# Optimization experiments

Measured on AMD Instinct MI355X. Metric: run time of the kernel, lower is better.

Reference implementation:

```python
import jax, jax.numpy as jnp
import numpy as np

NM, ND, E, H, HEADS = 1043, 2166, 512, 512, 8
EMM, EDD = 66752, 138624


def setup_inputs() -> dict:
    ks = iter(jax.random.split(jax.random.key(0), 64))
    def nk():
        return next(ks)
    s = 0.05
    inp = {
        'mirna_x': jax.random.normal(nk(), (NM, E), jnp.float32),
        'drug_x': jax.random.normal(nk(), (ND, E), jnp.float32),
    }
    for name, n, m in [('mm1', NM, EMM), ('mm2', NM, EMM), ('dd1', ND, EDD), ('dd2', ND, EDD)]:
        inp['edge_' + name] = jax.random.randint(nk(), (2, m), 0, n, jnp.int32)
        inp['attr_' + name] = jax.random.uniform(nk(), (m,), jnp.float32)
    for enc in ['m1', 'm2', 'd1', 'd2']:
        inp[enc + '_W1'] = jax.random.normal(nk(), (E, H), jnp.float32) * s
        inp[enc + '_b1'] = jax.random.normal(nk(), (H,), jnp.float32) * s
        inp[enc + '_W2'] = jax.random.normal(nk(), (H, H), jnp.float32) * s
        inp[enc + '_b2'] = jax.random.normal(nk(), (H,), jnp.float32) * s
    for p in ['mir', 'drug']:
        for w in ['Wq', 'Wk', 'Wv', 'Wo']:
            inp[p + '_' + w] = jax.random.normal(nk(), (E, E), jnp.float32) * s
        inp[p + '_fw'] = jax.random.normal(nk(), (4,), jnp.float32) * 0.5
        inp[p + '_fb'] = jax.random.normal(nk(), (1,), jnp.float32) * s
    return inp


def gcn_conv(x, W, b, edge, w):
    # PyG GCNConv: add self-loops (weight 1), symmetric normalization, aggregate at target.
    n = x.shape[0]
    h = x @ W
    loop = jnp.arange(n, dtype=edge.dtype)
    src = jnp.concatenate([edge[0], loop])
    dst = jnp.concatenate([edge[1], loop])
    ww = jnp.concatenate([w, jnp.ones((n,), w.dtype)])
    deg = jax.ops.segment_sum(ww, dst, num_segments=n)
    dis = jnp.where(deg > 0, jax.lax.rsqrt(deg), 0.0)
    norm = dis[src] * ww * dis[dst]  # [E+n]
    out = jax.ops.segment_sum(norm[:, None] * h[src], dst, num_segments=n)
    return out + b


def gcn_encoder(x, edge, w, W1, b1, W2, b2):
    x1 = jax.nn.relu(gcn_conv(x, W1, b1, edge, w))
    x2 = jax.nn.relu(gcn_conv(x1, W2, b2, edge, w))
    return jnp.concatenate([x1, x2], axis=1)  # [N, 2H]


def mha(x, Wq, Wk, Wv, Wo):
    # x: (views=4, N, E); attention over the N (num_features) axis, per view.
    V, N, _ = x.shape
    hd = E // HEADS
    def split(W):
        return (x @ W).reshape(V, N, HEADS, hd).transpose(0, 2, 1, 3)  # (V, h, N, hd)
    q, k, v = split(Wq), split(Wk), split(Wv)
    scores = jnp.einsum('vhnd,vhmd->vhnm', q, k) / jnp.sqrt(jnp.float32(hd))
    a = jax.nn.softmax(scores, axis=-1)
    o = jnp.einsum('vhnm,vhmd->vhnd', a, v).transpose(0, 2, 1, 3).reshape(V, N, E)
    return o @ Wo


def fuse(o, fw, fb):
    # 1x1 Conv2d over 4 channels -> weighted channel sum + bias, then view(E,-1).t()
    y = jnp.einsum('c,cne->ne', fw, o) + fb  # (N, E)
    return y.reshape(E, -1).T  # torch .view(out_channels, -1).t() on row-major data


def view_pipeline(v1, v2, Wq, Wk, Wv, Wo, fw, fb):
    emb = jnp.concatenate([v1, v2], axis=1)  # (N, 4E)
    N = emb.shape[0]
    # torch: .view(1, 4, E, -1) then transpose_(-1, -2) -> (4, N, E) after dropping batch dim
    x = emb.reshape(4, E, N).transpose(0, 2, 1)
    return fuse(mha(x, Wq, Wk, Wv, Wo), fw, fb)


def reference(mirna_x, drug_x, edge_mm1, attr_mm1, edge_mm2, attr_mm2, edge_dd1, attr_dd1, edge_dd2, attr_dd2, m1_W1, m1_b1, m1_W2, m1_b2, m2_W1, m2_b1, m2_W2, m2_b2, d1_W1, d1_b1, d1_W2, d1_b2, d2_W1, d2_b1, d2_W2, d2_b2, mir_Wq, mir_Wk, mir_Wv, mir_Wo, mir_fw, mir_fb, drug_Wq, drug_Wk, drug_Wv, drug_Wo, drug_fw, drug_fb):
    mv1 = gcn_encoder(mirna_x, edge_mm1, attr_mm1, m1_W1, m1_b1, m1_W2, m1_b2)
    mv2 = gcn_encoder(mirna_x, edge_mm2, attr_mm2, m2_W1, m2_b1, m2_W2, m2_b2)
    dv1 = gcn_encoder(drug_x, edge_dd1, attr_dd1, d1_W1, d1_b1, d1_W2, d1_b2)
    dv2 = gcn_encoder(drug_x, edge_dd2, attr_dd2, d2_W1, d2_b1, d2_W2, d2_b2)
    mir = view_pipeline(mv1, mv2, mir_Wq, mir_Wk, mir_Wv, mir_Wo, mir_fw, mir_fb)
    drg = view_pipeline(dv1, dv2, drug_Wq, drug_Wk, drug_Wv, drug_Wo, drug_fw, drug_fb)
    return mir @ drg.T  # (1043, 2166)
```

## Files before the change

### kernel.cpp

```cpp
#include <hip/hip_runtime.h>
#include <hip/hip_bf16.h>
#include <cmath>

#define NM 1043
#define ND 2166
#define ATT_SC 0.18033688011112042f

static inline int ceil_div(int a, int b) { return (a + b - 1) / b; }

typedef __attribute__((ext_vector_type(8))) short bf16x8;
typedef __attribute__((ext_vector_type(4))) float f32x4;
typedef __attribute__((ext_vector_type(2))) unsigned int u32x2;
typedef __attribute__((ext_vector_type(4))) unsigned int u32x4;

union U8 { u32x4 u; bf16x8 h; };

__device__ inline unsigned int pk2(float a, float b) {
  union { __hip_bfloat16 h; unsigned short u; } ca, cb;
  ca.h = __float2bfloat16(a);
  cb.h = __float2bfloat16(b);
  return (unsigned int)ca.u | ((unsigned int)cb.u << 16);
}

__device__ inline unsigned short bf1(float a) {
  union { __hip_bfloat16 h; unsigned short u; } c;
  c.h = __float2bfloat16(a);
  return c.u;
}

struct PrepW { const float* W[16]; unsigned short* Wt[16]; };

__global__ __launch_bounds__(256) void prep_w(PrepW p) {
  const int z = blockIdx.z;
  const float* __restrict__ W = p.W[z];
  unsigned short* __restrict__ Wt = p.Wt[z];
  const int n0 = blockIdx.x * 64, k0 = blockIdx.y * 64;
  __shared__ float Ws[64][65];
  const int tid = threadIdx.x;
#pragma unroll
  for (int it = 0; it < 16; it++) {
    int i = it * 256 + tid;
    int k = i >> 6, n = i & 63;
    Ws[k][n] = W[(size_t)(k0 + k) * 512 + n0 + n];
  }
  __syncthreads();
#pragma unroll
  for (int it = 0; it < 16; it++) {
    int i = it * 256 + tid;
    int n = i >> 6, k = i & 63;
    Wt[(size_t)(n0 + n) * 512 + k0 + k] = bf1(Ws[k][n]);
  }
}

struct BGemm {
  const void* A[6]; const unsigned short* Bt[6]; void* C[6];
  int M[6]; int lda[6]; float cs[6];
};

template<int AIN_BF16, int COUT_BF16>
__global__ __launch_bounds__(256) void gemm_mfma(BGemm g) {
  const int z = blockIdx.z;
  const int M = g.M[z];
  const int bm = blockIdx.y << 7;
  if (bm >= M) return;
  const int bn = blockIdx.x << 7;
  const int lda = g.lda[z];
  const float csc = g.cs[z];
  const char* __restrict__ Ab = (const char*)g.A[z];
  const char* __restrict__ Btb = (const char*)g.Bt[z];

  __shared__ short As_s[128 * 64];
  __shared__ short Bs_s[128 * 64];
  char* asb = (char*)As_s;
  char* bsb = (char*)Bs_s;

  const int tid = threadIdx.x;
  const int lane = tid & 63;
  const int w = tid >> 6;
  const int wm = (w >> 1) << 6, wn = (w & 1) << 6;
  const int fr = lane & 15, kg = lane >> 4;

  f32x4 acc[4][4];
#pragma unroll
  for (int i = 0; i < 4; i++)
#pragma unroll
    for (int j = 0; j < 4; j++) acc[i][j] = (f32x4){0.f, 0.f, 0.f, 0.f};

  for (int kb = 0; kb < 512; kb += 64) {
    __syncthreads();
#pragma unroll
    for (int qi = 0; qi < 4; qi++) {
      int qid = qi * 256 + tid;
      int mm = qid >> 3, qk = qid & 7;
      u32x4 wv = {0u, 0u, 0u, 0u};
      if (bm + mm < M) {
        if (AIN_BF16) {
          wv = *(const u32x4*)(Ab + ((size_t)(bm + mm) * lda + kb + qk * 8) * 2);
        } else {
          const float* ap = (const float*)Ab + (size_t)(bm + mm) * lda + kb + qk * 8;
          float4 f0 = ((const float4*)ap)[0];
          float4 f1 = ((const float4*)ap)[1];
          wv.x = pk2(f0.x, f0.y); wv.y = pk2(f0.z, f0.w);
          wv.z = pk2(f1.x, f1.y); wv.w = pk2(f1.z, f1.w);
        }
      }
      *(u32x4*)(asb + mm * 128 + ((qk * 16) ^ ((mm & 7) << 4))) = wv;
    }
#pragma unroll
    for (int qi = 0; qi < 4; qi++) {
      int qid = qi * 256 + tid;
      int nn = qid >> 3, qk = qid & 7;
      u32x4 bv = *(const u32x4*)(Btb + (((size_t)(bn + nn)) << 10) + (kb + qk * 8) * 2);
      *(u32x4*)(bsb + nn * 128 + ((qk * 16) ^ ((nn & 7) << 4))) = bv;
    }
    __syncthreads();

#pragma unroll
    for (int ks = 0; ks < 2; ks++) {
      bf16x8 af[4], bfv[4];
#pragma unroll
      for (int i = 0; i < 4; i++) {
        int row = wm + i * 16 + fr;
        af[i] = *(const bf16x8*)(asb + row * 128 + (((ks * 64) + kg * 16) ^ ((row & 7) << 4)));
      }
#pragma unroll
      for (int j = 0; j < 4; j++) {
        int row = wn + j * 16 + fr;
        bfv[j] = *(const bf16x8*)(bsb + row * 128 + (((ks * 64) + kg * 16) ^ ((row & 7) << 4)));
      }
#pragma unroll
      for (int i = 0; i < 4; i++)
#pragma unroll
        for (int j = 0; j < 4; j++)
          acc[i][j] = __builtin_amdgcn_mfma_f32_16x16x32_bf16(af[i], bfv[j], acc[i][j], 0, 0, 0);
    }
  }

#pragma unroll
  for (int i = 0; i < 4; i++) {
    int m0 = bm + wm + i * 16 + kg * 4;
#pragma unroll
    for (int j = 0; j < 4; j++) {
      int n = bn + wn + j * 16 + fr;
#pragma unroll
      for (int r = 0; r < 4; r++) {
        if (m0 + r < M) {
          float vv = acc[i][j][r] * csc;
          if (COUT_BF16) ((unsigned short*)g.C[z])[(size_t)(m0 + r) * 512 + n] = bf1(vv);
          else ((float*)g.C[z])[(size_t)(m0 + r) * 512 + n] = vv;
        }
      }
    }
  }
}

__global__ __launch_bounds__(256) void gemm_tn(
    const float* __restrict__ A, const float* __restrict__ B, float* __restrict__ C,
    int M, int N, int K, int lda, int ldb, int ldc) {
  __shared__ float As[16][65];
  __shared__ float Bs[16][65];
  const int tid = threadIdx.x;
  const int tx = tid & 15, ty = tid >> 4;
  const int bm = blockIdx.y << 6, bn = blockIdx.x << 6;
  float acc[4][4] = {};
  for (int k0 = 0; k0 < K; k0 += 16) {
    for (int i = tid; i < 16 * 64; i += 256) {
      int kk = i >> 6, mm = i & 63;
      int r = k0 + kk, c = bm + mm;
      As[kk][mm] = (r < K && c < M) ? A[(size_t)r * lda + c] : 0.f;
    }
    for (int i = tid; i < 16 * 64; i += 256) {
      int kk = i >> 6, nn = i & 63;
      int r = k0 + kk, c = bn + nn;
      Bs[kk][nn] = (r < K && c < N) ? B[(size_t)r * ldb + c] : 0.f;
    }
    __syncthreads();
#pragma unroll
    for (int kk = 0; kk < 16; kk++) {
      float a[4], b[4];
#pragma unroll
      for (int i = 0; i < 4; i++) a[i] = As[kk][ty + (i << 4)];
#pragma unroll
      for (int j = 0; j < 4; j++) b[j] = Bs[kk][tx + (j << 4)];
#pragma unroll
      for (int i = 0; i < 4; i++)
#pragma unroll
        for (int j = 0; j < 4; j++) acc[i][j] += a[i] * b[j];
    }
    __syncthreads();
  }
#pragma unroll
  for (int i = 0; i < 4; i++) {
    int r = bm + ty + (i << 4);
    if (r >= M) continue;
#pragma unroll
    for (int j = 0; j < 4; j++) {
      int c = bn + tx + (j << 4);
      if (c < N) C[(size_t)r * ldc + c] = acc[i][j];
    }
  }
}

struct DegB {
  const int* dst[4]; const float* attr[4];
  float* dis[4]; int* cnt[4];
  int epref[5];
};

__global__ __launch_bounds__(256) void deg_count_b(DegB g) {
  int et = blockIdx.x * 256 + threadIdx.x;
  if (et >= g.epref[4]) return;
  int z = (et >= g.epref[1]) + (et >= g.epref[2]) + (et >= g.epref[3]);
  int e = et - g.epref[z];
  int d = g.dst[z][e];
  atomicAdd(&g.dis[z][d], g.attr[z][e]);
  atomicAdd(&g.cnt[z][d], 1);
}

struct FinB { float* dis[4]; int n[4]; };

__global__ __launch_bounds__(256) void finish_dis_b(FinB g) {
  int z = blockIdx.z;
  int i = blockIdx.x * 256 + threadIdx.x;
  if (i < g.n[z]) g.dis[z][i] = rsqrtf(g.dis[z][i] + 1.0f);
}

struct ScanB { const int* cnt[4]; int* rowptr[4]; int n[4]; };

__global__ __launch_bounds__(256) void scan_b(ScanB s) {
  int z = blockIdx.x;
  int n = s.n[z];
  const int* cnt = s.cnt[z];
  int* rp = s.rowptr[z];
  __shared__ int sums[256];
  int tid = threadIdx.x;
  int chunk = (n + 255) >> 8;
  int start = tid * chunk;
  int local = 0;
  for (int i = 0; i < chunk; i++) {
    int idx = start + i;
    if (idx < n) local += cnt[idx];
  }
  sums[tid] = local;
  __syncthreads();
  for (int off = 1; off < 256; off <<= 1) {
    int t = (tid >= off) ? sums[tid - off] : 0;
    __syncthreads();
    sums[tid] += t;
    __syncthreads();
  }
  int base = sums[tid] - local;
  int total = sums[255];
  int run = base;
  for (int i = 0; i < chunk; i++) {
    int idx = start + i;
    if (idx < n) { rp[idx] = run; run += cnt[idx]; }
  }
  if (tid == 0) rp[n] = total;
}

struct FillB {
  const int* src[4]; const int* dst[4]; const float* attr[4];
  const int* rowptr[4]; int* cur[4]; int* col[4]; float* val[4];
  int epref[5];
};

__global__ __launch_bounds__(256) void fill_b(FillB f) {
  int et = blockIdx.x * 256 + threadIdx.x;
  if (et >= f.epref[4]) return;
  int z = (et >= f.epref[1]) + (et >= f.epref[2]) + (et >= f.epref[3]);
  int e = et - f.epref[z];
  int d = f.dst[z][e];
  int pos = f.rowptr[z][d] + atomicAdd(&f.cur[z][d], 1);
  f.col[z][pos] = f.src[z][e];
  f.val[z][pos] = f.attr[z][e];
}

struct GathB {
  const int* rowptr[4]; const int* col[4]; const float* val[4];
  const float* dis[4]; const float* h[4]; const float* b[4];
  float* out[4]; int n[4];
};

__global__ __launch_bounds__(256) void gcn_gather_b(GathB c) {
  const int z = blockIdx.z;
  const int node = blockIdx.x;
  if (node >= c.n[z]) return;
  const int tid = threadIdx.x;
  const int* __restrict__ col = c.col[z];
  const float* __restrict__ val = c.val[z];
  const float* __restrict__ dis = c.dis[z];
  const float* __restrict__ h = c.h[z];
  const int beg = c.rowptr[z][node], end = c.rowptr[z][node + 1];
  float acc0 = 0.f, acc1 = 0.f;
  int e = beg;
  for (; e + 4 <= end; e += 4) {
    int s0 = col[e], s1 = col[e + 1], s2 = col[e + 2], s3 = col[e + 3];
    float w0 = val[e] * dis[s0];
    float w1 = val[e + 1] * dis[s1];
    float w2 = val[e + 2] * dis[s2];
    float w3 = val[e + 3] * dis[s3];
    const float* p0 = h + ((size_t)s0 << 9);
    const float* p1 = h + ((size_t)s1 << 9);
    const float* p2 = h + ((size_t)s2 << 9);
    const float* p3 = h + ((size_t)s3 << 9);
    acc0 += w0 * p0[tid] + w1 * p1[tid] + w2 * p2[tid] + w3 * p3[tid];
    acc1 += w0 * p0[tid + 256] + w1 * p1[tid + 256] + w2 * p2[tid + 256] + w3 * p3[tid + 256];
  }
  for (; e < end; e++) {
    int s = col[e];
    float w = val[e] * dis[s];
    const float* p = h + ((size_t)s << 9);
    acc0 += w * p[tid];
    acc1 += w * p[tid + 256];
  }
  const float dd = dis[node];
  const float* hp = h + ((size_t)node << 9);
  float o0 = fmaxf(dd * acc0 + dd * dd * hp[tid] + c.b[z][tid], 0.f);
  float o1 = fmaxf(dd * acc1 + dd * dd * hp[tid + 256] + c.b[z][tid + 256], 0.f);
  float* op = c.out[z] + (size_t)node * 2048;
  op[tid] = o0;
  op[tid + 256] = o1;
}

struct GatherB { const float* emb[2]; float* xv[2]; int n[2]; };

__global__ __launch_bounds__(256) void gather_b(GatherB g) {
  int z = blockIdx.z;
  int n = g.n[z];
  size_t i = (size_t)blockIdx.x * 256 + threadIdx.x;
  if (i >= (size_t)n * 2048) return;
  int e = (int)(i & 511);
  size_t t = i >> 9;
  int v = (int)(t / n);
  int nn = (int)(t - (size_t)v * n);
  g.xv[z][i] = g.emb[z][((size_t)v * 512 + e) * n + nn];
}

struct AttArgs {
  const unsigned short* Q[2]; const unsigned short* K[2]; const unsigned short* V[2];
  unsigned short* O[2]; int N[2];
};

__global__ __launch_bounds__(256) void attn6_kernel(AttArgs ar) {
  const int z = blockIdx.z;
  const int N = ar.N[z];
  const int qb = blockIdx.x * 128;
  if (qb >= N) return;
  const int vh = blockIdx.y, v = vh >> 3, h = vh & 7;
  const size_t base = (size_t)v * N * 512 + (size_t)h * 64;
  const unsigned short* __restrict__ Qb = ar.Q[z] + base;
  const char* __restrict__ Kc = (const char*)(ar.K[z] + base);
  const char* __restrict__ Vc = (const char*)(ar.V[z] + base);
  unsigned short* __restrict__ Ob = ar.O[z] + base;

  __shared__ short kt_s[64 * 64];
  __shared__ short vt_s[64 * 64];
  char* ktb = (char*)kt_s;
  char* vtb = (char*)vt_s;

  const int tid = threadIdx.x;
  const int lane = tid & 63;
  const int w = tid >> 6;
  const int a15 = lane & 15;
  const int g = lane >> 4;

  const int qA = qb + w * 32 + a15;
  const int qB = qA + 16;
  bf16x8 qfA0 = {}, qfA1 = {}, qfB0 = {}, qfB1 = {};
  if (qA < N) {
    qfA0 = *(const bf16x8*)(Qb + (size_t)qA * 512 + g * 8);
    qfA1 = *(const bf16x8*)(Qb + (size_t)qA * 512 + 32 + g * 8);
  }
  if (qB < N) {
    qfB0 = *(const bf16x8*)(Qb + (size_t)qB * 512 + g * 8);
    qfB1 = *(const bf16x8*)(Qb + (size_t)qB * 512 + 32 + g * 8);
  }

  float rmA = -INFINITY, rsA = 0.f, rmB = -INFINITY, rsB = 0.f;
  f32x4 oA0 = {0.f, 0.f, 0.f, 0.f}, oA1 = oA0, oA2 = oA0, oA3 = oA0;
  f32x4 oB0 = oA0, oB1 = oA0, oB2 = oA0, oB3 = oA0;

  const int swzk = (a15 & 7) << 4;
  const int swzv = a15 << 3;
  const int skr = tid >> 2, skq = (tid & 3) * 16;
  const int vsr = tid & 15, vsc = tid >> 4;

  for (int kb = 0; kb < N; kb += 64) {
    __syncthreads();
    {
      const int sw = (skr & 7) << 4;
      const char* kp = Kc + (size_t)(kb + skr) * 1024;
      u32x4 k0 = {0u,0u,0u,0u}, k1 = {0u,0u,0u,0u};
      if (kb + skr < N) {
        k0 = *(const u32x4*)(kp + skq);
        k1 = *(const u32x4*)(kp + skq + 64);
      }
      *(u32x4*)(ktb + skr * 128 + (skq ^ sw)) = k0;
      *(u32x4*)(ktb + skr * 128 + ((skq + 64) ^ sw)) = k1;
    }
    {
      const int r0 = kb + 4 * vsr;
      u32x2 i0 = {0u,0u}, i1 = {0u,0u}, i2 = {0u,0u}, i3 = {0u,0u};
      const char* vp = Vc + (size_t)r0 * 1024 + vsc * 8;
      if (r0 + 0 < N) i0 = *(const u32x2*)(vp);
      if (r0 + 1 < N) i1 = *(const u32x2*)(vp + 1024);
      if (r0 + 2 < N) i2 = *(const u32x2*)(vp + 2048);
      if (r0 + 3 < N) i3 = *(const u32x2*)(vp + 3072);
      const int dd = 4 * vsc, kby = 8 * vsr;
      u32x2 o;
      o.x = (i0.x & 0xFFFFu) | (i1.x << 16); o.y = (i2.x & 0xFFFFu) | (i3.x << 16);
      *(u32x2*)(vtb + (dd + 0) * 128 + (kby ^ (((dd + 0) & 15) << 3))) = o;
      o.x = (i0.x >> 16) | (i1.x & 0xFFFF0000u); o.y = (i2.x >> 16) | (i3.x & 0xFFFF0000u);
      *(u32x2*)(vtb + (dd + 1) * 128 + (kby ^ (((dd + 1) & 15) << 3))) = o;
      o.x = (i0.y & 0xFFFFu) | (i1.y << 16); o.y = (i2.y & 0xFFFFu) | (i3.y << 16);
      *(u32x2*)(vtb + (dd + 2) * 128 + (kby ^ (((dd + 2) & 15) << 3))) = o;
      o.x = (i0.y >> 16) | (i1.y & 0xFFFF0000u); o.y = (i2.y >> 16) | (i3.y & 0xFFFF0000u);
      *(u32x2*)(vtb + (dd + 3) * 128 + (kby ^ (((dd + 3) & 15) << 3))) = o;
    }
    __syncthreads();

    f32x4 sA0 = {0.f,0.f,0.f,0.f}, sA1 = sA0, sA2 = sA0, sA3 = sA0;
    f32x4 sB0 = sA0, sB1 = sA0, sB2 = sA0, sB3 = sA0;
#define QK2(m, sAm, sBm, s2, qfa, qfb) { \
    bf16x8 kf = *(const bf16x8*)(ktb + (16 * m + a15) * 128 + ((64 * s2 + 16 * g) ^ swzk)); \
    sAm = __builtin_amdgcn_mfma_f32_16x16x32_bf16(kf, qfa, sAm, 0, 0, 0); \
    sBm = __builtin_amdgcn_mfma_f32_16x16x32_bf16(kf, qfb, sBm, 0, 0, 0); }
    QK2(0, sA0, sB0, 0, qfA0, qfB0) QK2(1, sA1, sB1, 0, qfA0, qfB0)
    QK2(2, sA2, sB2, 0, qfA0, qfB0) QK2(3, sA3, sB3, 0, qfA0, qfB0)
    QK2(0, sA0, sB0, 1, qfA1, qfB1) QK2(1, sA1, sB1, 1, qfA1, qfB1)
    QK2(2, sA2, sB2, 1, qfA1, qfB1) QK2(3, sA3, sB3, 1, qfA1, qfB1)
#undef QK2

    if (kb + 64 > N) {
#define MSK(sfm, sgm, m) { int kk = kb + 16 * m + 4 * g; \
      if (kk + 0 >= N) { sfm.x = -INFINITY; sgm.x = -INFINITY; } \
      if (kk + 1 >= N) { sfm.y = -INFINITY; sgm.y = -INFINITY; } \
      if (kk + 2 >= N) { sfm.z = -INFINITY; sgm.z = -INFINITY; } \
      if (kk + 3 >= N) { sfm.w = -INFINITY; sgm.w = -INFINITY; } }
      MSK(sA0, sB0, 0) MSK(sA1, sB1, 1) MSK(sA2, sB2, 2) MSK(sA3, sB3, 3)
#undef MSK
    }

#define SMX(sfm, px, py) { \
    float e0 = exp2f(sfm.x - nm), e1 = exp2f(sfm.y - nm); \
    float e2 = exp2f(sfm.z - nm), e3 = exp2f(sfm.w - nm); \
    ps += (e0 + e1) + (e2 + e3); \
    px = pk2(e0, e1); py = pk2(e2, e3); }
#define PV(md, om, s2, pbr) { \
    const char* vr = vtb + (16 * md + a15) * 128; \
    u32x2 v0 = *(const u32x2*)(vr + ((64 * s2 + 8 * g) ^ swzv)); \
    u32x2 v1 = *(const u32x2*)(vr + ((64 * s2 + 32 + 8 * g) ^ swzv)); \
    U8 av; av.u.x = v0.x; av.u.y = v0.y; av.u.z = v1.x; av.u.w = v1.y; \
    om = __builtin_amdgcn_mfma_f32_16x16x32_bf16(av.h, pbr, om, 0, 0, 0); }
#define SOFTMAX_PV(sf0, sf1, sf2, sf3, rm, rs, q0, q1, q2, q3) { \
    float tmax = fmaxf(fmaxf(fmaxf(sf0.x, sf0.y), fmaxf(sf0.z, sf0.w)), \
                       fmaxf(fmaxf(sf1.x, sf1.y), fmaxf(sf1.z, sf1.w))); \
    tmax = fmaxf(tmax, fmaxf(fmaxf(fmaxf(sf2.x, sf2.y), fmaxf(sf2.z, sf2.w)), \
                             fmaxf(fmaxf(sf3.x, sf3.y), fmaxf(sf3.z, sf3.w)))); \
    tmax = fmaxf(tmax, __shfl_xor(tmax, 16)); \
    tmax = fmaxf(tmax, __shfl_xor(tmax, 32)); \
    const float nm = fmaxf(rm, tmax); \
    const float sc = exp2f(rm - nm); \
    float ps = 0.f; \
    U8 pb0, pb1; \
    SMX(sf0, pb0.u.x, pb0.u.y) SMX(sf1, pb0.u.z, pb0.u.w) \
    SMX(sf2, pb1.u.x, pb1.u.y) SMX(sf3, pb1.u.z, pb1.u.w) \
    ps += __shfl_xor(ps, 16); \
    ps += __shfl_xor(ps, 32); \
    rs = rs * sc + ps; \
    rm = nm; \
    q0 *= sc; q1 *= sc; q2 *= sc; q3 *= sc; \
    PV(0, q0, 0, pb0.h) PV(1, q1, 0, pb0.h) PV(2, q2, 0, pb0.h) PV(3, q3, 0, pb0.h) \
    PV(0, q0, 1, pb1.h) PV(1, q1, 1, pb1.h) PV(2, q2, 1, pb1.h) PV(3, q3, 1, pb1.h) }

    SOFTMAX_PV(sA0, sA1, sA2, sA3, rmA, rsA, oA0, oA1, oA2, oA3)
    SOFTMAX_PV(sB0, sB1, sB2, sB3, rmB, rsB, oB0, oB1, oB2, oB3)
#undef SOFTMAX_PV
#undef PV
#undef SMX
  }

  if (qA < N) {
    const float inv = 1.0f / rsA;
    char* op = (char*)(Ob + (size_t)qA * 512) + g * 8;
    u32x2 r;
    r.x = pk2(oA0.x * inv, oA0.y * inv); r.y = pk2(oA0.z * inv, oA0.w * inv);
    *(u32x2*)(op) = r;
    r.x = pk2(oA1.x * inv, oA1.y * inv); r.y = pk2(oA1.z * inv, oA1.w * inv);
    *(u32x2*)(op + 32) = r;
    r.x = pk2(oA2.x * inv, oA2.y * inv); r.y = pk2(oA2.z * inv, oA2.w * inv);
    *(u32x2*)(op + 64) = r;
    r.x = pk2(oA3.x * inv, oA3.y * inv); r.y = pk2(oA3.z * inv, oA3.w * inv);
    *(u32x2*)(op + 96) = r;
  }
  if (qB < N) {
    const float inv = 1.0f / rsB;
    char* op = (char*)(Ob + (size_t)qB * 512) + g * 8;
    u32x2 r;
    r.x = pk2(oB0.x * inv, oB0.y * inv); r.y = pk2(oB0.z * inv, oB0.w * inv);
    *(u32x2*)(op) = r;
    r.x = pk2(oB1.x * inv, oB1.y * inv); r.y = pk2(oB1.z * inv, oB1.w * inv);
    *(u32x2*)(op + 32) = r;
    r.x = pk2(oB2.x * inv, oB2.y * inv); r.y = pk2(oB2.z * inv, oB2.w * inv);
    *(u32x2*)(op + 64) = r;
    r.x = pk2(oB3.x * inv, oB3.y * inv); r.y = pk2(oB3.z * inv, oB3.w * inv);
    *(u32x2*)(op + 96) = r;
  }
}

struct FuseB { const float* mha[2]; const float* fw[2]; const float* fb[2]; float* y[2]; int n[2]; };

__global__ __launch_bounds__(256) void fuse_b(FuseB fz) {
  int z = blockIdx.z;
  int n = fz.n[z];
  int i = blockIdx.x * 256 + threadIdx.x;
  if (i >= n * 512) return;
  size_t stride = (size_t)n * 512;
  const float* m = fz.mha[z];
  const float* fw = fz.fw[z];
  float acc = fz.fb[z][0];
  acc += fw[0] * m[i];
  acc += fw[1] * m[stride + i];
  acc += fw[2] * m[2 * stride + i];
  acc += fw[3] * m[3 * stride + i];
  fz.y[z][i] = acc;
}

extern "C" void kernel_launch(void* const* d_in, const int* in_sizes, int n_in,
                              void* d_out, int out_size, void* d_ws, size_t ws_size,
                              hipStream_t stream) {
  const float* mirna_x = (const float*)d_in[0];
  const float* drug_x  = (const float*)d_in[1];
  const int* edge[4] = { (const int*)d_in[2], (const int*)d_in[4], (const int*)d_in[6], (const int*)d_in[8] };
  const float* attr[4] = { (const float*)d_in[3], (const float*)d_in[5], (const float*)d_in[7], (const float*)d_in[9] };
  const int m[4] = { in_sizes[2] / 2, in_sizes[4] / 2, in_sizes[6] / 2, in_sizes[8] / 2 };
  const int nn4[4] = { NM, NM, ND, ND };
  float* out = (float*)d_out;

  float* ws = (float*)d_ws;
  size_t off = 0;
  auto take = [&](size_t nelem) {
    float* r = ws + off;
    off += (nelem + 255) & ~(size_t)255;
    return r;
  };
  const size_t HN = (size_t)NM * 512, HD = (size_t)ND * 512;
  const size_t HALL = 2 * HN + 2 * HD;
  float* emb_m = take((size_t)NM * 2048);
  float* emb_d = take((size_t)ND * 2048);
  float* region = take(2 * HALL);
  float* h4[4] = { region, region + HN, region + 2 * HN, region + 2 * HN + HD };
  float* xv_m = region;
  float* xv_d = region + (size_t)NM * 2048;
  float* dis_all = take(4 * 2560);
  float* dis4[4] = { dis_all, dis_all + 2560, dis_all + 2 * 2560, dis_all + 3 * 2560 };
  int* cnt_all = (int*)take(4 * 2560);
  int* cnt4[4] = { cnt_all, cnt_all + 2560, cnt_all + 2 * 2560, cnt_all + 3 * 2560 };
  int* rp_all = (int*)take(4 * 2304);
  int* rp4[4] = { rp_all, rp_all + 2304, rp_all + 2 * 2304, rp_all + 3 * 2304 };
  int* col4[4];
  float* val4[4];
  for (int z = 0; z < 4; z++) {
    col4[z] = (int*)take(m[z]);
    val4[z] = take(m[z]);
  }
  unsigned short* Qm = (unsigned short*)take((size_t)NM * 1024);
  unsigned short* Km = (unsigned short*)take((size_t)NM * 1024);
  unsigned short* Vm = (unsigned short*)take((size_t)NM * 1024);
  unsigned short* Qd = (unsigned short*)take((size_t)ND * 1024);
  unsigned short* Kd = (unsigned short*)take((size_t)ND * 1024);
  unsigned short* Vd = (unsigned short*)take((size_t)ND * 1024);
  float* mha_m = take((size_t)NM * 2048);
  float* mha_d = take((size_t)ND * 2048);
  float* y_m = take(HN);
  float* y_d = take(HD);
  unsigned short* wt = (unsigned short*)take((size_t)16 * 131072);

  int pref = 0;
  int epref[5];
  for (int z = 0; z < 4; z++) { epref[z] = pref; pref += m[z]; }
  epref[4] = pref;

  PrepW pw;
  for (int z = 0; z < 4; z++) {
    pw.W[z] = (const float*)d_in[10 + 4 * z];
    pw.W[4 + z] = (const float*)d_in[12 + 4 * z];
    pw.W[8 + z] = (const float*)d_in[26 + z];
    pw.W[12 + z] = (const float*)d_in[32 + z];
  }
  for (int z = 0; z < 16; z++) pw.Wt[z] = wt + (size_t)z * 262144;
  prep_w<<<dim3(8, 8, 16), 256, 0, stream>>>(pw);

  hipMemsetAsync(dis_all, 0, 4 * 2560 * sizeof(float), stream);
  hipMemsetAsync(cnt_all, 0, 4 * 2560 * sizeof(int), stream);

  DegB db;
  for (int z = 0; z < 4; z++) {
    db.dst[z] = edge[z] + m[z]; db.attr[z] = attr[z];
    db.dis[z] = dis4[z]; db.cnt[z] = cnt4[z];
  }
  for (int z = 0; z < 5; z++) db.epref[z] = epref[z];
  deg_count_b<<<ceil_div(pref, 256), 256, 0, stream>>>(db);

  FinB fn;
  for (int z = 0; z < 4; z++) { fn.dis[z] = dis4[z]; fn.n[z] = nn4[z]; }
  finish_dis_b<<<dim3(ceil_div(ND, 256), 1, 4), 256, 0, stream>>>(fn);

  ScanB sb;
  for (int z = 0; z < 4; z++) { sb.cnt[z] = cnt4[z]; sb.rowptr[z] = rp4[z]; sb.n[z] = nn4[z]; }
  scan_b<<<4, 256, 0, stream>>>(sb);

  hipMemsetAsync(cnt_all, 0, 4 * 2560 * sizeof(int), stream);
  FillB fl;
  for (int z = 0; z < 4; z++) {
    fl.src[z] = edge[z]; fl.dst[z] = edge[z] + m[z]; fl.attr[z] = attr[z];
    fl.rowptr[z] = rp4[z]; fl.cur[z] = cnt4[z]; fl.col[z] = col4[z]; fl.val[z] = val4[z];
  }
  for (int z = 0; z < 5; z++) fl.epref[z] = epref[z];
  fill_b<<<ceil_div(pref, 256), 256, 0, stream>>>(fl);

  BGemm c1;
  const float* xin[4] = { mirna_x, mirna_x, drug_x, drug_x };
  for (int z = 0; z < 6; z++) c1.cs[z] = 1.0f;
  for (int z = 0; z < 4; z++) {
    c1.A[z] = xin[z]; c1.Bt[z] = wt + (size_t)z * 262144; c1.C[z] = h4[z];
    c1.M[z] = nn4[z]; c1.lda[z] = 512;
  }
  for (int z = 4; z < 6; z++) { c1.A[z] = nullptr; c1.Bt[z] = nullptr; c1.C[z] = nullptr; c1.M[z] = 0; c1.lda[z] = 512; }
  gemm_mfma<0, 0><<<dim3(4, ceil_div(ND, 128), 4), 256, 0, stream>>>(c1);

  float* embp[4] = { emb_m, emb_m + 1024, emb_d, emb_d + 1024 };
  GathB g1;
  for (int z = 0; z < 4; z++) {
    g1.rowptr[z] = rp4[z]; g1.col[z] = col4[z]; g1.val[z] = val4[z];
    g1.dis[z] = dis4[z]; g1.h[z] = h4[z]; g1.b[z] = (const float*)d_in[11 + 4 * z];
    g1.out[z] = embp[z]; g1.n[z] = nn4[z];
  }
  gcn_gather_b<<<dim3(ND, 1, 4), 256, 0, stream>>>(g1);

  BGemm c2 = c1;
  for (int z = 0; z < 4; z++) {
    c2.A[z] = embp[z]; c2.Bt[z] = wt + (size_t)(4 + z) * 262144; c2.C[z] = h4[z];
    c2.M[z] = nn4[z]; c2.lda[z] = 2048;
  }
  gemm_mfma<0, 0><<<dim3(4, ceil_div(ND, 128), 4), 256, 0, stream>>>(c2);

  GathB g2 = g1;
  for (int z = 0; z < 4; z++) { g2.b[z] = (const float*)d_in[13 + 4 * z]; g2.out[z] = embp[z] + 512; }
  gcn_gather_b<<<dim3(ND, 1, 4), 256, 0, stream>>>(g2);

  GatherB gt;
  gt.emb[0] = emb_m; gt.emb[1] = emb_d; gt.xv[0] = xv_m; gt.xv[1] = xv_d;
  gt.n[0] = NM; gt.n[1] = ND;
  gather_b<<<dim3(ceil_div(ND * 2048, 256), 1, 2), 256, 0, stream>>>(gt);

  BGemm qkv;
  unsigned short* qkvc[6] = { Qm, Km, Vm, Qd, Kd, Vd };
  for (int z = 0; z < 6; z++) {
    qkv.A[z] = (z < 3) ? xv_m : xv_d;
    qkv.Bt[z] = wt + (size_t)((z < 3) ? (8 + z) : (12 + z - 3)) * 262144;
    qkv.C[z] = qkvc[z];
    qkv.M[z] = (z < 3) ? 4 * NM : 4 * ND; qkv.lda[z] = 512;
    qkv.cs[z] = (z == 0 || z == 3) ? ATT_SC : 1.0f;
  }
  gemm_mfma<0, 1><<<dim3(4, ceil_div(4 * ND, 128), 6), 256, 0, stream>>>(qkv);

  AttArgs aa;
  aa.Q[0] = Qm; aa.K[0] = Km; aa.V[0] = Vm; aa.O[0] = (unsigned short*)xv_m; aa.N[0] = NM;
  aa.Q[1] = Qd; aa.K[1] = Kd; aa.V[1] = Vd; aa.O[1] = (unsigned short*)xv_d; aa.N[1] = ND;
  attn6_kernel<<<dim3(ceil_div(ND, 128), 32, 2), 256, 0, stream>>>(aa);

  BGemm wo;
  for (int z = 0; z < 6; z++) wo.cs[z] = 1.0f;
  for (int z = 0; z < 2; z++) {
    wo.A[z] = (z == 0) ? xv_m : xv_d;
    wo.Bt[z] = wt + (size_t)(z == 0 ? 11 : 15) * 262144;
    wo.C[z] = (z == 0) ? mha_m : mha_d;
    wo.M[z] = (z == 0) ? 4 * NM : 4 * ND; wo.lda[z] = 512;
  }
  for (int z = 2; z < 6; z++) { wo.A[z] = nullptr; wo.Bt[z] = nullptr; wo.C[z] = nullptr; wo.M[z] = 0; wo.lda[z] = 512; }
  gemm_mfma<1, 0><<<dim3(4, ceil_div(4 * ND, 128), 2), 256, 0, stream>>>(wo);

  FuseB fz;
  fz.mha[0] = mha_m; fz.mha[1] = mha_d;
  fz.fw[0] = (const float*)d_in[30]; fz.fw[1] = (const float*)d_in[36];
  fz.fb[0] = (const float*)d_in[31]; fz.fb[1] = (const float*)d_in[37];
  fz.y[0] = y_m; fz.y[1] = y_d;
  fz.n[0] = NM; fz.n[1] = ND;
  fuse_b<<<dim3(ceil_div(ND * 512, 256), 1, 2), 256, 0, stream>>>(fz);

  gemm_tn<<<dim3(ceil_div(ND, 64), ceil_div(NM, 64)), 256, 0, stream>>>(
      y_m, y_d, out, NM, ND, 512, NM, ND, ND);
}
```

Measured before the change: 839.8 us.

## Use bf16 MFMA for final GEMM and double-buffer K/V tiles in attention

Replaces the scalar fp32 final mir@drug^T GEMM with a bf16 MFMA kernel, adding a transpose-and-convert pass that lays y out row-major in bf16. Separately, the attention kernel now double-buffers K/V tiles in shared memory, issuing global loads for the next tile before computing on the current one. The aim is to cut FMA-bound GEMM time and hide global-load latency in attention, at the cost of bf16 rounding in the output GEMM and double the attention LDS footprint.

```diff
diff --git a/kernel.cpp b/kernel.cpp
--- a/kernel.cpp
+++ b/kernel.cpp
@@ -49,6 +49,32 @@
     int i = it * 256 + tid;
     int n = i >> 6, k = i & 63;
     Wt[(size_t)(n0 + n) * 512 + k0 + k] = bf1(Ws[k][n]);
+  }
+}
+
+struct PrepYT { const float* y[2]; unsigned short* yT[2]; int n[2]; };
+
+__global__ __launch_bounds__(256) void prep_yt(PrepYT p) {
+  const int z = blockIdx.z;
+  const int n = p.n[z];
+  const int i0 = blockIdx.x * 64, k0 = blockIdx.y * 64;
+  if (i0 >= n) return;
+  const float* __restrict__ y = p.y[z];
+  unsigned short* __restrict__ yT = p.yT[z];
+  __shared__ float T[64][65];
+  const int tid = threadIdx.x;
+#pragma unroll
+  for (int it = 0; it < 16; it++) {
+    int idx = it * 256 + tid;
+    int kk = idx >> 6, ii = idx & 63;
+    T[kk][ii] = (i0 + ii < n) ? y[(size_t)(k0 + kk) * n + i0 + ii] : 0.f;
+  }
+  __syncthreads();
+#pragma unroll
+  for (int it = 0; it < 16; it++) {
+    int idx = it * 256 + tid;
+    int ii = idx >> 6, kk = idx & 63;
+    if (i0 + ii < n) yT[(size_t)(i0 + ii) * 512 + k0 + kk] = bf1(T[kk][ii]);
   }
 }
 
@@ -154,49 +180,81 @@
   }
 }
 
-__global__ __launch_bounds__(256) void gemm_tn(
-    const float* __restrict__ A, const float* __restrict__ B, float* __restrict__ C,
-    int M, int N, int K, int lda, int ldb, int ldc) {
-  __shared__ float As[16][65];
-  __shared__ float Bs[16][65];
+__global__ __launch_bounds__(256) void gemm_tn2(const unsigned short* __restrict__ Am,
+                                                const unsigned short* __restrict__ Bn,
+                                                float* __restrict__ C, int M, int N) {
+  const int bm = blockIdx.y << 7;
+  const int bn = blockIdx.x << 7;
+  __shared__ short As_s[128 * 64];
+  __shared__ short Bs_s[128 * 64];
+  char* asb = (char*)As_s;
+  char* bsb = (char*)Bs_s;
   const int tid = threadIdx.x;
-  const int tx = tid & 15, ty = tid >> 4;
-  const int bm = blockIdx.y << 6, bn = blockIdx.x << 6;
-  float acc[4][4] = {};
-  for (int k0 = 0; k0 < K; k0 += 16) {
-    for (int i = tid; i < 16 * 64; i += 256) {
-      int kk = i >> 6, mm = i & 63;
-      int r = k0 + kk, c = bm + mm;
-      As[kk][mm] = (r < K && c < M) ? A[(size_t)r * lda + c] : 0.f;
-    }
-    for (int i = tid; i < 16 * 64; i += 256) {
-      int kk = i >> 6, nn = i & 63;
-      int r = k0 + kk, c = bn + nn;
-      Bs[kk][nn] = (r < K && c < N) ? B[(size_t)r * ldb + c] : 0.f;
-    }
+  const int lane = tid & 63;
+  const int w = tid >> 6;
+  const int wm = (w >> 1) << 6, wn = (w & 1) << 6;
+  const int fr = lane & 15, kg = lane >> 4;
+
+  f32x4 acc[4][4];
+#pragma unroll
+  for (int i = 0; i < 4; i++)
+#pragma unroll
+    for (int j = 0; j < 4; j++) acc[i][j] = (f32x4){0.f, 0.f, 0.f, 0.f};
+
+  for (int kb = 0; kb < 512; kb += 64) {
     __syncthreads();
 #pragma unroll
-    for (int kk = 0; kk < 16; kk++) {
-      float a[4], b[4];
-#pragma unroll
-      for (int i = 0; i < 4; i++) a[i] = As[kk][ty + (i << 4)];
-#pragma unroll
-      for (int j = 0; j < 4; j++) b[j] = Bs[kk][tx + (j << 4)];
+    for (int qi = 0; qi < 4; qi++) {
+      int qid = qi * 256 + tid;
+      int mm = qid >> 3, qk = qid & 7;
+      u32x4 wv = {0u, 0u, 0u, 0u};
+      if (bm + mm < M)
+        wv = *(const u32x4*)((const char*)Am + ((size_t)(bm + mm) * 512 + kb + qk * 8) * 2);
+      *(u32x4*)(asb + mm * 128 + ((qk * 16) ^ ((mm & 7) << 4))) = wv;
+    }
+#pragma unroll
+    for (int qi = 0; qi < 4; qi++) {
+      int qid = qi * 256 + tid;
+      int nn = qid >> 3, qk = qid & 7;
+      u32x4 bv = {0u, 0u, 0u, 0u};
+      if (bn + nn < N)
+        bv = *(const u32x4*)((const char*)Bn + ((size_t)(bn + nn) * 512 + kb + qk * 8) * 2);
+      *(u32x4*)(bsb + nn * 128 + ((qk * 16) ^ ((nn & 7) << 4))) = bv;
+    }
+    __syncthreads();
+
+#pragma unroll
+    for (int ks = 0; ks < 2; ks++) {
+      bf16x8 af[4], bfv[4];
+#pragma unroll
+      for (int i = 0; i < 4; i++) {
+        int row = wm + i * 16 + fr;
+        af[i] = *(const bf16x8*)(asb + row * 128 + (((ks * 64) + kg * 16) ^ ((row & 7) << 4)));
+      }
+#pragma unroll
+      for (int j = 0; j < 4; j++) {
+        int row = wn + j * 16 + fr;
+        bfv[j] = *(const bf16x8*)(bsb + row * 128 + (((ks * 64) + kg * 16) ^ ((row & 7) << 4)));
+      }
 #pragma unroll
       for (int i = 0; i < 4; i++)
 #pragma unroll
-        for (int j = 0; j < 4; j++) acc[i][j] += a[i] * b[j];
-    }
-    __syncthreads();
-  }
+        for (int j = 0; j < 4; j++)
+          acc[i][j] = __builtin_amdgcn_mfma_f32_16x16x32_bf16(af[i], bfv[j], acc[i][j], 0, 0, 0);
+    }
+  }
+
 #pragma unroll
   for (int i = 0; i < 4; i++) {
-    int r = bm + ty + (i << 4);
-    if (r >= M) continue;
+    int m0 = bm + wm + i * 16 + kg * 4;
 #pragma unroll
     for (int j = 0; j < 4; j++) {
-      int c = bn + tx + (j << 4);
-      if (c < N) C[(size_t)r * ldc + c] = acc[i][j];
+      int n = bn + wn + j * 16 + fr;
+      if (n >= N) continue;
+#pragma unroll
+      for (int r = 0; r < 4; r++) {
+        if (m0 + r < M) C[(size_t)(m0 + r) * N + n] = acc[i][j][r];
+      }
     }
   }
 }
@@ -342,7 +400,7 @@
   unsigned short* O[2]; int N[2];
 };
 
-__global__ __launch_bounds__(256) void attn6_kernel(AttArgs ar) {
+__global__ __launch_bounds__(256) void attn7_kernel(AttArgs ar) {
   const int z = blockIdx.z;
   const int N = ar.N[z];
   const int qb = blockIdx.x * 128;
@@ -354,16 +412,14 @@
   const char* __restrict__ Vc = (const char*)(ar.V[z] + base);
   unsigned short* __restrict__ Ob = ar.O[z] + base;
 
-  __shared__ short kt_s[64 * 64];
-  __shared__ short vt_s[64 * 64];
-  char* ktb = (char*)kt_s;
-  char* vtb = (char*)vt_s;
+  __shared__ short kt_s[2][64 * 64];
+  __shared__ short vt_s[2][64 * 64];
 
   const int tid = threadIdx.x;
   const int lane = tid & 63;
   const int w = tid >> 6;
   const int a15 = lane & 15;
-  const int g = lane >> 4;
+  const int g = tid >> 4 & 3;
 
   const int qA = qb + w * 32 + a15;
   const int qB = qA + 16;
@@ -386,39 +442,53 @@
   const int skr = tid >> 2, skq = (tid & 3) * 16;
   const int vsr = tid & 15, vsc = tid >> 4;
 
-  for (int kb = 0; kb < N; kb += 64) {
-    __syncthreads();
-    {
-      const int sw = (skr & 7) << 4;
+  u32x4 k0r = {0u,0u,0u,0u}, k1r = {0u,0u,0u,0u};
+  u32x2 v0r = {0u,0u}, v1r = {0u,0u}, v2r = {0u,0u}, v3r = {0u,0u};
+
+  auto load_tile = [&](int kb) {
+    k0r = (u32x4){0u,0u,0u,0u}; k1r = k0r;
+    if (kb + skr < N) {
       const char* kp = Kc + (size_t)(kb + skr) * 1024;
-      u32x4 k0 = {0u,0u,0u,0u}, k1 = {0u,0u,0u,0u};
-      if (kb + skr < N) {
-        k0 = *(const u32x4*)(kp + skq);
-        k1 = *(const u32x4*)(kp + skq + 64);
-      }
-      *(u32x4*)(ktb + skr * 128 + (skq ^ sw)) = k0;
-      *(u32x4*)(ktb + skr * 128 + ((skq + 64) ^ sw)) = k1;
-    }
-    {
-      const int r0 = kb + 4 * vsr;
-      u32x2 i0 = {0u,0u}, i1 = {0u,0u}, i2 = {0u,0u}, i3 = {0u,0u};
-      const char* vp = Vc + (size_t)r0 * 1024 + vsc * 8;
-      if (r0 + 0 < N) i0 = *(const u32x2*)(vp);
-      if (r0 + 1 < N) i1 = *(const u32x2*)(vp + 1024);
-      if (r0 + 2 < N) i2 = *(const u32x2*)(vp + 2048);
-      if (r0 + 3 < N) i3 = *(const u32x2*)(vp + 3072);
-      const int dd = 4 * vsc, kby = 8 * vsr;
-      u32x2 o;
-      o.x = (i0.x & 0xFFFFu) | (i1.x << 16); o.y = (i2.x & 0xFFFFu) | (i3.x << 16);
-      *(u32x2*)(vtb + (dd + 0) * 128 + (kby ^ (((dd + 0) & 15) << 3))) = o;
-      o.x = (i0.x >> 16) | (i1.x & 0xFFFF0000u); o.y = (i2.x >> 16) | (i3.x & 0xFFFF0000u);
-      *(u32x2*)(vtb + (dd + 1) * 128 + (kby ^ (((dd + 1) & 15) << 3))) = o;
-      o.x = (i0.y & 0xFFFFu) | (i1.y << 16); o.y = (i2.y & 0xFFFFu) | (i3.y << 16);
-      *(u32x2*)(vtb + (dd + 2) * 128 + (kby ^ (((dd + 2) & 15) << 3))) = o;
-      o.x = (i0.y >> 16) | (i1.y & 0xFFFF0000u); o.y = (i2.y >> 16) | (i3.y & 0xFFFF0000u);
-      *(u32x2*)(vtb + (dd + 3) * 128 + (kby ^ (((dd + 3) & 15) << 3))) = o;
-    }
-    __syncthreads();
+      k0r = *(const u32x4*)(kp + skq);
+      k1r = *(const u32x4*)(kp + skq + 64);
+    }
+    const int r0 = kb + 4 * vsr;
+    const char* vp = Vc + (size_t)r0 * 1024 + vsc * 8;
+    v0r = (u32x2){0u,0u}; v1r = v0r; v2r = v0r; v3r = v0r;
+    if (r0 + 0 < N) v0r = *(const u32x2*)(vp);
+    if (r0 + 1 < N) v1r = *(const u32x2*)(vp + 1024);
+    if (r0 + 2 < N) v2r = *(const u32x2*)(vp + 2048);
+    if (r0 + 3 < N) v3r = *(const u32x2*)(vp + 3072);
+  };
+  auto write_tile = [&](int buf) {
+    char* ktb = (char*)kt_s[buf];
+    char* vtb = (char*)vt_s[buf];
+    const int sw = (skr & 7) << 4;
+    *(u32x4*)(ktb + skr * 128 + (skq ^ sw)) = k0r;
+    *(u32x4*)(ktb + skr * 128 + ((skq + 64) ^ sw)) = k1r;
+    const int dd = 4 * vsc, kby = 8 * vsr;
+    u32x2 o;
+    o.x = (v0r.x & 0xFFFFu) | (v1r.x << 16); o.y = (v2r.x & 0xFFFFu) | (v3r.x << 16);
+    *(u32x2*)(vtb + (dd + 0) * 128 + (kby ^ (((dd + 0) & 15) << 3))) = o;
+    o.x = (v0r.x >> 16) | (v1r.x & 0xFFFF0000u); o.y = (v2r.x >> 16) | (v3r.x & 0xFFFF0000u);
+    *(u32x2*)(vtb + (dd + 1) * 128 + (kby ^ (((dd + 1) & 15) << 3))) = o;
+    o.x = (v0r.y & 0xFFFFu) | (v1r.y << 16); o.y = (v2r.y & 0xFFFFu) | (v3r.y << 16);
+    *(u32x2*)(vtb + (dd + 2) * 128 + (kby ^ (((dd + 2) & 15) << 3))) = o;
+    o.x = (v0r.y >> 16) | (v1r.y & 0xFFFF0000u); o.y = (v2r.y >> 16) | (v3r.y & 0xFFFF0000u);
+    *(u32x2*)(vtb + (dd + 3) * 128 + (kby ^ (((dd + 3) & 15) << 3))) = o;
+  };
+
+  const int nt = (N + 63) >> 6;
+  load_tile(0);
+  write_tile(0);
+  __syncthreads();
+
+  for (int t = 0; t < nt; t++) {
+    const int kb = t << 6;
+    if (t + 1 < nt) load_tile(kb + 64);
+
+    const char* ktb = (const char*)kt_s[t & 1];
+    const char* vtb = (const char*)vt_s[t & 1];
 
     f32x4 sA0 = {0.f,0.f,0.f,0.f}, sA1 = sA0, sA2 = sA0, sA3 = sA0;
     f32x4 sB0 = sA0, sB1 = sA0, sB2 = sA0, sB3 = sA0;
@@ -479,6 +549,12 @@
 #undef SOFTMAX_PV
 #undef PV
 #undef SMX
+
+    __syncthreads();
+    if (t + 1 < nt) {
+      write_tile((t + 1) & 1);
+      __syncthreads();
+    }
   }
 
   if (qA < N) {
@@ -575,6 +651,8 @@
   float* mha_d = take((size_t)ND * 2048);
   float* y_m = take(HN);
   float* y_d = take(HD);
+  unsigned short* yT_m = (unsigned short*)take((size_t)NM * 256);
+  unsigned short* yT_d = (unsigned short*)take((size_t)ND * 256);
   unsigned short* wt = (unsigned short*)take((size_t)16 * 131072);
 
   int pref = 0;
@@ -669,7 +747,7 @@
   AttArgs aa;
   aa.Q[0] = Qm; aa.K[0] = Km; aa.V[0] = Vm; aa.O[0] = (unsigned short*)xv_m; aa.N[0] = NM;
   aa.Q[1] = Qd; aa.K[1] = Kd; aa.V[1] = Vd; aa.O[1] = (unsigned short*)xv_d; aa.N[1] = ND;
-  attn6_kernel<<<dim3(ceil_div(ND, 128), 32, 2), 256, 0, stream>>>(aa);
+  attn7_kernel<<<dim3(ceil_div(ND, 128), 32, 2), 256, 0, stream>>>(aa);
 
   BGemm wo;
   for (int z = 0; z < 6; z++) wo.cs[z] = 1.0f;
@@ -690,6 +768,12 @@
   fz.n[0] = NM; fz.n[1] = ND;
   fuse_b<<<dim3(ceil_div(ND * 512, 256), 1, 2), 256, 0, stream>>>(fz);
 
-  gemm_tn<<<dim3(ceil_div(ND, 64), ceil_div(NM, 64)), 256, 0, stream>>>(
-      y_m, y_d, out, NM, ND, 512, NM, ND, ND);
-}
+  PrepYT pyt;
+  pyt.y[0] = y_m; pyt.y[1] = y_d;
+  pyt.yT[0] = yT_m; pyt.yT[1] = yT_d;
+  pyt.n[0] = NM; pyt.n[1] = ND;
+  prep_yt<<<dim3(ceil_div(ND, 64), 8, 2), 256, 0, stream>>>(pyt);
+
+  gemm_tn2<<<dim3(ceil_div(ND, 128), ceil_div(NM, 128)), 256, 0, stream>>>(
+      yT_m, yT_d, out, NM, ND);
+}
```

New measurement: 724.0 us. 1.16x faster.
